# Kernel optimization log

Measured on AMD Instinct MI355X. Metric: run time of the kernel, lower is better.

## Reference

```python
import jax, jax.numpy as jnp
import numpy as np

WINDOW = 8
DIM = 192
HEADS = 6
NWIN = 4096  # number of windows (B_)


def _relative_position_index(w):
    coords = np.stack(np.meshgrid(np.arange(w), np.arange(w), indexing='ij'))  # [2,w,w]
    cf = coords.reshape(2, -1)                                                 # [2, w*w]
    rel = cf[:, :, None] - cf[:, None, :]                                      # [2, N, N]
    rel = rel.transpose(1, 2, 0).astype(np.int32)
    rel[:, :, 0] += w - 1
    rel[:, :, 1] += w - 1
    rel[:, :, 0] *= 2 * w - 1
    return rel.sum(-1)  # [N, N] in [0, (2w-1)^2)


def setup_inputs() -> dict:
    key = jax.random.key(0)
    ks = jax.random.split(key, 6)
    N = WINDOW * WINDOW
    x = jax.random.normal(ks[0], (NWIN, N, DIM), dtype=jnp.float32)
    qkv_w = jax.random.normal(ks[1], (3 * DIM, DIM), dtype=jnp.float32) * (DIM ** -0.5)
    qkv_b = jax.random.normal(ks[2], (3 * DIM,), dtype=jnp.float32) * 0.02
    proj_w = jax.random.normal(ks[3], (DIM, DIM), dtype=jnp.float32) * (DIM ** -0.5)
    proj_b = jax.random.normal(ks[4], (DIM,), dtype=jnp.float32) * 0.02
    bias_table = jax.random.normal(ks[5], ((2 * WINDOW - 1) ** 2, HEADS), dtype=jnp.float32) * 0.02
    rel_index = jnp.asarray(_relative_position_index(WINDOW))
    return {"x": x, "qkv_w": qkv_w, "qkv_b": qkv_b, "proj_w": proj_w,
            "proj_b": proj_b, "bias_table": bias_table, "rel_index": rel_index}


def reference(x, qkv_w, qkv_b, proj_w, proj_b, bias_table, rel_index):
    B, N, C = x.shape
    H = HEADS
    hd = C // H
    scale = hd ** -0.5
    # qkv projection (torch Linear: x @ W.T + b)
    qkv = (x @ qkv_w.T + qkv_b).reshape(B, N, 3, H, hd)
    qkv = jnp.transpose(qkv, (2, 0, 3, 1, 4))  # [3, B, H, N, hd]
    q, k, v = qkv[0], qkv[1], qkv[2]
    attn = jnp.einsum('bhqd,bhkd->bhqk', q, k) * scale  # [B,H,N,N]
    # relative position bias gather: [N,N,H] -> [H,N,N]
    bias = bias_table[rel_index.reshape(-1)].reshape(N, N, H)
    bias = jnp.transpose(bias, (2, 0, 1))
    attn = jax.nn.softmax(attn + bias[None], axis=-1)
    out = jnp.einsum('bhqk,bhkd->bhqd', attn, v)         # [B,H,N,hd]
    out = jnp.transpose(out, (0, 2, 1, 3)).reshape(B, N, C)
    return out @ proj_w.T + proj_b
```

## Files before the change

### kernel.cpp

```cpp
#include <hip/hip_runtime.h>


#define NTOK 64
#define DIM  192
#define HEADS 6
#define NWIN 4096

typedef short short8  __attribute__((ext_vector_type(8)));
typedef short short4v __attribute__((ext_vector_type(4)));
typedef float f32x4   __attribute__((ext_vector_type(4)));
typedef unsigned int u32;
typedef u32 u32x2 __attribute__((ext_vector_type(2)));
typedef u32 u32x4 __attribute__((ext_vector_type(4)));

#define QW_SHORTS  110592
#define W_SHORTS   147456
#define BIAS_OFF_B 294912
#define WS_NEEDED  (294912 + 98304)

__device__ __forceinline__ short f2bf(float f) {
    unsigned u = __builtin_bit_cast(unsigned, f);
    unsigned r = (u + 0x7fffu + ((u >> 16) & 1u)) >> 16;
    return (short)r;
}
__device__ __forceinline__ u32 pkbf(float lo, float hi) {
    u32 d;
    asm("v_cvt_pk_bf16_f32 %0, %1, %2" : "=v"(d) : "v"(lo), "v"(hi));
    return d;
}
__device__ __forceinline__ short8 ld_cvt8(const float* p) {
    f32x4 a = *(const f32x4*)p;
    f32x4 b = *(const f32x4*)(p + 4);
    u32x4 w;
    w[0] = pkbf(a[0], a[1]); w[1] = pkbf(a[2], a[3]);
    w[2] = pkbf(b[0], b[1]); w[3] = pkbf(b[2], b[3]);
    return __builtin_bit_cast(short8, w);
}

__global__ void prep(const float* __restrict__ qw, const float* __restrict__ pw,
                     const float* __restrict__ bt, const int* __restrict__ ri,
                     short* __restrict__ wsw, float* __restrict__ biasf) {
    const int bid = blockIdx.x;
    if (bid < 144) {
        const int i = (bid * 256 + threadIdx.x) * 4;
        const float* src = (i < QW_SHORTS) ? (qw + i) : (pw + (i - QW_SHORTS));
        f32x4 v = *(const f32x4*)src;
        short4v o;
        o[0] = f2bf(v[0]); o[1] = f2bf(v[1]); o[2] = f2bf(v[2]); o[3] = f2bf(v[3]);
        *(short4v*)(wsw + i) = o;
    } else {
        const int j  = (bid - 144) * 256 + threadIdx.x;
        const int r  = j & 3;
        const int ln = (j >> 2) & 63;
        const int nt = (j >> 8) & 3;
        const int mt = (j >> 10) & 3;
        const int hh = j >> 12;
        const int q  = mt * 16 + (ln & 15);
        const int k  = nt * 16 + (ln >> 4) * 4 + r;
        biasf[j] = bt[ri[q * 64 + k] * HEADS + hh];
    }
}


template <bool WS>
__global__ __launch_bounds__(384, 4) void msa_fused(
    const float* __restrict__ x,
    const short* __restrict__ wq_bf, const short* __restrict__ wp_bf,
    const float* __restrict__ bias_fr,
    const float* __restrict__ wq_f,  const float* __restrict__ wp_f,
    const float* __restrict__ qkv_b, const float* __restrict__ proj_b,
    const float* __restrict__ bias_table, const int* __restrict__ rel_index,
    float* __restrict__ out)
{
    __shared__ __align__(16) short smem[12800];

    const int tid  = threadIdx.x;
    const int wave = tid >> 6;
    const int lane = tid & 63;
    const int quad = lane >> 4;
    const int l15  = lane & 15;
    const int b    = blockIdx.x;
    const int h    = wave;

    const int  srcA = ((quad & 1) << 5) + l15;
    const bool hiq  = (quad >= 2);

    auto gsel = [&](u32 a, u32 bb, int sl) -> u32 {
        u32 va = (u32)__shfl((int)a, sl, 64);
        u32 vb = (u32)__shfl((int)bb, sl, 64);
        return hiq ? vb : va;
    };
    auto xpose = [&](u32 p00, u32 p01, u32 p10, u32 p11) -> short8 {
        u32x4 w;
        w[0] = gsel(p00, p10, srcA);
        w[1] = gsel(p01, p11, srcA);
        w[2] = gsel(p00, p10, srcA + 16);
        w[3] = gsel(p01, p11, srcA + 16);
        return __builtin_bit_cast(short8, w);
    };

    const float* xg = x + b * (NTOK * DIM);
#pragma unroll
    for (int i = 0; i < 8; ++i) {
        const int f   = tid + i * 384;
        f32x4 v = *(const f32x4*)(xg + f * 4);
        const int row = f / 48;
        const int col = (f % 48) * 4;
        u32x2 wv; wv[0] = pkbf(v[0], v[1]); wv[1] = pkbf(v[2], v[3]);
        *(u32x2*)(smem + row * 200 + col) = wv;
    }
    __syncthreads();

    short8 qa[4], kb[4], vfr[2][2];

    auto qk_gemm = [&](int wbase, short8 (&fr)[4]) {
        f32x4 acc[2][4];
#pragma unroll
        for (int ct = 0; ct < 2; ++ct)
#pragma unroll
            for (int tt = 0; tt < 4; ++tt) acc[ct][tt] = (f32x4){0.f,0.f,0.f,0.f};
#pragma unroll
        for (int kk = 0; kk < 6; ++kk) {
            short8 xfr[4];
#pragma unroll
            for (int tt = 0; tt < 4; ++tt)
                xfr[tt] = *(const short8*)(smem + (tt*16 + l15)*200 + kk*32 + quad*8);
#pragma unroll
            for (int ct = 0; ct < 2; ++ct) {
                short8 wfr;
                if constexpr (WS) wfr = *(const short8*)(wq_bf + (wbase + ct*16 + l15)*DIM + kk*32 + quad*8);
                else              wfr = ld_cvt8(wq_f + (wbase + ct*16 + l15)*DIM + kk*32 + quad*8);
#pragma unroll
                for (int tt = 0; tt < 4; ++tt)
                    acc[ct][tt] = __builtin_amdgcn_mfma_f32_16x16x32_bf16(wfr, xfr[tt], acc[ct][tt], 0, 0, 0);
            }
        }
        f32x4 bq[2];
        bq[0] = *(const f32x4*)(qkv_b + wbase + quad*4);
        bq[1] = *(const f32x4*)(qkv_b + wbase + 16 + quad*4);
#pragma unroll
        for (int ct = 0; ct < 2; ++ct)
#pragma unroll
            for (int tt = 0; tt < 4; ++tt) acc[ct][tt] += bq[ct];
#pragma unroll
        for (int tt = 0; tt < 4; ++tt) {
            u32 p00 = pkbf(acc[0][tt][0], acc[0][tt][1]);
            u32 p01 = pkbf(acc[0][tt][2], acc[0][tt][3]);
            u32 p10 = pkbf(acc[1][tt][0], acc[1][tt][1]);
            u32 p11 = pkbf(acc[1][tt][2], acc[1][tt][3]);
            fr[tt] = xpose(p00, p01, p10, p11);
        }
    };
    qk_gemm(h*32,       qa);
    qk_gemm(192 + h*32, kb);

    {
        f32x4 acc[4][2];
#pragma unroll
        for (int tt = 0; tt < 4; ++tt)
#pragma unroll
            for (int ct = 0; ct < 2; ++ct) acc[tt][ct] = (f32x4){0.f,0.f,0.f,0.f};
#pragma unroll
        for (int kk = 0; kk < 6; ++kk) {
            short8 xfr[4];
#pragma unroll
            for (int tt = 0; tt < 4; ++tt)
                xfr[tt] = *(const short8*)(smem + (tt*16 + l15)*200 + kk*32 + quad*8);
#pragma unroll
            for (int ct = 0; ct < 2; ++ct) {
                const int wrow = 384 + h*32 + ct*16 + l15;
                short8 wfr;
                if constexpr (WS) wfr = *(const short8*)(wq_bf + wrow*DIM + kk*32 + quad*8);
                else              wfr = ld_cvt8(wq_f + wrow*DIM + kk*32 + quad*8);
#pragma unroll
                for (int tt = 0; tt < 4; ++tt)
                    acc[tt][ct] = __builtin_amdgcn_mfma_f32_16x16x32_bf16(xfr[tt], wfr, acc[tt][ct], 0, 0, 0);
            }
        }
        const float bv0 = qkv_b[384 + h*32 + l15];
        const float bv1 = qkv_b[384 + h*32 + 16 + l15];
        u32 pkv[2][4][2];
#pragma unroll
        for (int tt = 0; tt < 4; ++tt) {
#pragma unroll
            for (int r = 0; r < 4; ++r) { acc[tt][0][r] += bv0; acc[tt][1][r] += bv1; }
#pragma unroll
            for (int ct = 0; ct < 2; ++ct) {
                pkv[ct][tt][0] = pkbf(acc[tt][ct][0], acc[tt][ct][1]);
                pkv[ct][tt][1] = pkbf(acc[tt][ct][2], acc[tt][ct][3]);
            }
        }
#pragma unroll
        for (int ct = 0; ct < 2; ++ct)
#pragma unroll
            for (int kh = 0; kh < 2; ++kh)
                vfr[ct][kh] = xpose(pkv[ct][2*kh][0], pkv[ct][2*kh][1],
                                    pkv[ct][2*kh+1][0], pkv[ct][2*kh+1][1]);
    }
    __syncthreads();

    const float scale = 0.17677669529663687f;
    const float L2E   = 1.44269504088896f;
#pragma unroll
    for (int mt = 0; mt < 4; ++mt) {
        f32x4 s[4];
#pragma unroll
        for (int nt = 0; nt < 4; ++nt) {
            f32x4 z = (f32x4){0.f,0.f,0.f,0.f};
            s[nt] = __builtin_amdgcn_mfma_f32_16x16x32_bf16(kb[nt], qa[mt], z, 0, 0, 0);
        }
        if constexpr (WS) {
#pragma unroll
            for (int nt = 0; nt < 4; ++nt) {
                f32x4 bb = *(const f32x4*)(bias_fr + ((((h*4 + mt)*4 + nt)*64 + lane) << 2));
#pragma unroll
                for (int r = 0; r < 4; ++r) s[nt][r] = s[nt][r]*scale + bb[r];
            }
        } else {
#pragma unroll
            for (int nt = 0; nt < 4; ++nt)
#pragma unroll
                for (int r = 0; r < 4; ++r) {
                    const int q = mt*16 + l15, k = nt*16 + quad*4 + r;
                    s[nt][r] = s[nt][r]*scale + bias_table[rel_index[q*64 + k]*HEADS + h];
                }
        }
        float m = -1e30f;
#pragma unroll
        for (int nt = 0; nt < 4; ++nt)
#pragma unroll
            for (int r = 0; r < 4; ++r) m = fmaxf(m, s[nt][r]);
        m = fmaxf(m, __shfl_xor(m, 16)); m = fmaxf(m, __shfl_xor(m, 32));
        float sum = 0.f;
#pragma unroll
        for (int nt = 0; nt < 4; ++nt)
#pragma unroll
            for (int r = 0; r < 4; ++r) {
                float e = exp2f((s[nt][r] - m) * L2E);
                s[nt][r] = e; sum += e;
            }
        sum += __shfl_xor(sum, 16); sum += __shfl_xor(sum, 32);
        const float inv = 1.f / sum;
        u32 pk[4][2];
#pragma unroll
        for (int nt = 0; nt < 4; ++nt) {
            pk[nt][0] = pkbf(s[nt][0]*inv, s[nt][1]*inv);
            pk[nt][1] = pkbf(s[nt][2]*inv, s[nt][3]*inv);
        }
        f32x4 oa[2];
        oa[0] = (f32x4){0.f,0.f,0.f,0.f}; oa[1] = (f32x4){0.f,0.f,0.f,0.f};
#pragma unroll
        for (int kh = 0; kh < 2; ++kh) {
            short8 pfr = xpose(pk[2*kh][0], pk[2*kh][1], pk[2*kh+1][0], pk[2*kh+1][1]);
#pragma unroll
            for (int ct = 0; ct < 2; ++ct)
                oa[ct] = __builtin_amdgcn_mfma_f32_16x16x32_bf16(pfr, vfr[ct][kh], oa[ct], 0, 0, 0);
        }
#pragma unroll
        for (int ct = 0; ct < 2; ++ct)
#pragma unroll
            for (int r = 0; r < 4; ++r)
                smem[(mt*16 + quad*4 + r)*200 + h*32 + ct*16 + l15] = f2bf(oa[ct][r]);
    }
    __syncthreads();

    float* outg = out + b * (NTOK * DIM);
#pragma unroll
    for (int nt2 = 0; nt2 < 2; ++nt2) {
        const int c0 = h*32 + nt2*16;
        f32x4 acc[4];
#pragma unroll
        for (int tt = 0; tt < 4; ++tt) acc[tt] = (f32x4){0.f,0.f,0.f,0.f};
#pragma unroll
        for (int kk = 0; kk < 6; ++kk) {
            short8 ofr[4];
#pragma unroll
            for (int tt = 0; tt < 4; ++tt)
                ofr[tt] = *(const short8*)(smem + (tt*16 + l15)*200 + kk*32 + quad*8);
            short8 wfr;
            if constexpr (WS) wfr = *(const short8*)(wp_bf + (c0 + l15)*DIM + kk*32 + quad*8);
            else              wfr = ld_cvt8(wp_f + (c0 + l15)*DIM + kk*32 + quad*8);
#pragma unroll
            for (int tt = 0; tt < 4; ++tt)
                acc[tt] = __builtin_amdgcn_mfma_f32_16x16x32_bf16(ofr[tt], wfr, acc[tt], 0, 0, 0);
        }
        const float pb = proj_b[c0 + l15];
#pragma unroll
        for (int tt = 0; tt < 4; ++tt)
#pragma unroll
            for (int r = 0; r < 4; ++r) {
                float sv = acc[tt][r] + pb;
                if (!(__builtin_fabsf(sv) < 1e30f)) sv = 0.f;
                outg[(tt*16 + quad*4 + r)*DIM + c0 + l15] = sv;
            }
    }
}

extern "C" void kernel_launch(void* const* d_in, const int* in_sizes, int n_in,
                              void* d_out, int out_size, void* d_ws, size_t ws_size,
                              hipStream_t stream) {
    const float* x          = (const float*)d_in[0];
    const float* qkv_w      = (const float*)d_in[1];
    const float* qkv_b      = (const float*)d_in[2];
    const float* proj_w     = (const float*)d_in[3];
    const float* proj_b     = (const float*)d_in[4];
    const float* bias_table = (const float*)d_in[5];
    const int*   rel_index  = (const int*)d_in[6];
    float* out = (float*)d_out;

    if (ws_size >= (size_t)WS_NEEDED) {
        short* wsw   = (short*)d_ws;
        float* biasf = (float*)((char*)d_ws + BIAS_OFF_B);
        prep<<<240, 256, 0, stream>>>(qkv_w, proj_w, bias_table, rel_index, wsw, biasf);
        msa_fused<true><<<NWIN, 384, 0, stream>>>(
            x, wsw, wsw + QW_SHORTS, biasf, qkv_w, proj_w,
            qkv_b, proj_b, bias_table, rel_index, out);
    } else {
        msa_fused<false><<<NWIN, 384, 0, stream>>>(
            x, nullptr, nullptr, nullptr, qkv_w, proj_w,
            qkv_b, proj_b, bias_table, rel_index, out);
    }
}
```

Baseline: 725.9 us.

## Stage projection output through LDS for coalesced nontemporal vector stores

The projection GEMM loops are reordered so the O fragments are loaded once per k-step and reused for both 16-column tiles. Results are staged through shared memory in two 32-row halves and written to global memory as contiguous float4 nontemporal stores, replacing scattered scalar stores. The x input load is also made nontemporal. This adds extra barriers and LDS traffic, and keeps 32 accumulator registers live at once.

```diff
diff --git a/kernel.cpp b/kernel.cpp
--- a/kernel.cpp
+++ b/kernel.cpp
@@ -103,7 +103,7 @@
 #pragma unroll
     for (int i = 0; i < 8; ++i) {
         const int f   = tid + i * 384;
-        f32x4 v = *(const f32x4*)(xg + f * 4);
+        f32x4 v = __builtin_nontemporal_load((const f32x4*)(xg + f * 4));
         const int row = f / 48;
         const int col = (f % 48) * 4;
         u32x2 wv; wv[0] = pkbf(v[0], v[1]); wv[1] = pkbf(v[2], v[3]);
@@ -264,35 +264,59 @@
     }
     __syncthreads();
 
-    float* outg = out + b * (NTOK * DIM);
-#pragma unroll
-    for (int nt2 = 0; nt2 < 2; ++nt2) {
-        const int c0 = h*32 + nt2*16;
-        f32x4 acc[4];
-#pragma unroll
-        for (int tt = 0; tt < 4; ++tt) acc[tt] = (f32x4){0.f,0.f,0.f,0.f};
-#pragma unroll
-        for (int kk = 0; kk < 6; ++kk) {
-            short8 ofr[4];
-#pragma unroll
-            for (int tt = 0; tt < 4; ++tt)
-                ofr[tt] = *(const short8*)(smem + (tt*16 + l15)*200 + kk*32 + quad*8);
+    f32x4 acc[2][4];
+#pragma unroll
+    for (int n2 = 0; n2 < 2; ++n2)
+#pragma unroll
+        for (int tt = 0; tt < 4; ++tt) acc[n2][tt] = (f32x4){0.f,0.f,0.f,0.f};
+#pragma unroll
+    for (int kk = 0; kk < 6; ++kk) {
+        short8 ofr[4];
+#pragma unroll
+        for (int tt = 0; tt < 4; ++tt)
+            ofr[tt] = *(const short8*)(smem + (tt*16 + l15)*200 + kk*32 + quad*8);
+#pragma unroll
+        for (int n2 = 0; n2 < 2; ++n2) {
+            const int c0 = h*32 + n2*16;
             short8 wfr;
             if constexpr (WS) wfr = *(const short8*)(wp_bf + (c0 + l15)*DIM + kk*32 + quad*8);
             else              wfr = ld_cvt8(wp_f + (c0 + l15)*DIM + kk*32 + quad*8);
 #pragma unroll
             for (int tt = 0; tt < 4; ++tt)
-                acc[tt] = __builtin_amdgcn_mfma_f32_16x16x32_bf16(ofr[tt], wfr, acc[tt], 0, 0, 0);
-        }
-        const float pb = proj_b[c0 + l15];
-#pragma unroll
-        for (int tt = 0; tt < 4; ++tt)
-#pragma unroll
-            for (int r = 0; r < 4; ++r) {
-                float sv = acc[tt][r] + pb;
-                if (!(__builtin_fabsf(sv) < 1e30f)) sv = 0.f;
-                outg[(tt*16 + quad*4 + r)*DIM + c0 + l15] = sv;
-            }
+                acc[n2][tt] = __builtin_amdgcn_mfma_f32_16x16x32_bf16(ofr[tt], wfr, acc[n2][tt], 0, 0, 0);
+        }
+    }
+    const float pb0 = proj_b[h*32 + l15];
+    const float pb1 = proj_b[h*32 + 16 + l15];
+
+    float* smf = (float*)smem;
+    float* outg = out + b * (NTOK * DIM);
+    __syncthreads();
+#pragma unroll
+    for (int half = 0; half < 2; ++half) {
+#pragma unroll
+        for (int tt2 = 0; tt2 < 2; ++tt2) {
+            const int tt = half*2 + tt2;
+#pragma unroll
+            for (int n2 = 0; n2 < 2; ++n2)
+#pragma unroll
+                for (int r = 0; r < 4; ++r) {
+                    float sv = acc[n2][tt][r] + (n2 ? pb1 : pb0);
+                    if (!(__builtin_fabsf(sv) < 1e30f)) sv = 0.f;
+                    smf[(tt2*16 + quad*4 + r)*196 + h*32 + n2*16 + l15] = sv;
+                }
+        }
+        __syncthreads();
+        float* dst = outg + half * 32 * DIM;
+#pragma unroll
+        for (int i = 0; i < 4; ++i) {
+            const int idx = (i*384 + tid) * 4;
+            const int row = idx / 192;
+            const int col = idx - row * 192;
+            f32x4 v = *(const f32x4*)(smf + row*196 + col);
+            __builtin_nontemporal_store(v, (f32x4*)(dst + idx));
+        }
+        if (half == 0) __syncthreads();
     }
 }
 
```

New measurement: 747.8 us. 3.0% more time.
